# Kernel tuning notes

Hardware: AMD Instinct MI355X
Metric: run time of the kernel (lower is better)

The kernel has to match this reference:

```python
import jax, jax.numpy as jnp
import numpy as np

B, S, BITS = 1024, 4096, 32

# Boolean gates expressed as float arithmetic on {0,1} pulses (exact for 0/1 inputs,
# matching the SNN gate semantics: AND=a*b, OR=a+b-ab, NOT=1-a, XOR=a+b-2ab).

def _and(a, b):
    return a * b

def _or(a, b):
    return a + b - a * b

def _not(a):
    return 1.0 - a

def _xor(a, b):
    return a + b - 2.0 * a * b

def _full_adder(a, b, c):
    axb = _xor(a, b)
    s = _xor(axb, c)
    # carry = (a AND b) OR ((a XOR b) AND c); the two terms are disjoint for booleans
    carry = a * b + axb * c
    return s, carry


def setup_inputs() -> dict:
    key = jax.random.key(0)
    # FP32 bit-pulses: x[..., 0]=sign, x[..., 1:9]=exponent (MSB first), x[..., 9:32]=mantissa
    x = jax.random.bernoulli(key, 0.5, (B, S, BITS)).astype(jnp.float32)
    return {"x": x}


def reference(x):
    e_x = x[..., 1:9]    # exponent bits, MSB first  [.., 8]
    m_x = x[..., 9:32]   # mantissa bits, MSB first  [.., 23]
    ones = jnp.ones(x.shape[:-1] + (1,), dtype=x.dtype)

    # shift = e_x - 127 via ripple subtract: e + NOT(127) + 1.
    # NOT(127) in MSB-first 8-bit is [1,0,0,0,0,0,0,0].
    borrow = ones
    shift = [None] * 8
    for i in range(7, -1, -1):
        nb = 1.0 if i == 0 else 0.0
        s, borrow = _full_adder(e_x[..., i:i + 1], nb, borrow)
        shift[i] = s
    s_bits = shift                      # MSB first
    s_inv = [_not(b) for b in s_bits]

    # high 5 bits (s0..s4) all zero
    hi_zero = s_inv[0]
    for i in range(1, 5):
        hi_zero = _and(hi_zero, s_inv[i])

    is_0 = _and(hi_zero, _and(s_inv[5], _and(s_inv[6], s_inv[7])))
    is_1 = _and(hi_zero, _and(s_inv[5], _and(s_inv[6], s_bits[7])))
    is_2 = _and(hi_zero, _and(s_inv[5], _and(s_bits[6], s_inv[7])))
    is_3 = _and(hi_zero, _and(s_inv[5], _and(s_bits[6], s_bits[7])))
    is_4 = _and(hi_zero, _and(s_bits[5], _and(s_inv[6], s_inv[7])))
    is_s = [is_0, is_1, is_2, is_3, is_4]

    m = [m_x[..., i:i + 1] for i in range(4)]  # top 4 mantissa bits (MSB first)

    final_bits = []
    for b in range(5):
        terms = []
        for s in range(5):
            if s == b:
                terms.append(_and(is_s[s], ones))
            elif s > b:
                m_idx = s - 1 - b
                if m_idx < 4:
                    terms.append(_and(is_s[s], m[m_idx]))
        res = terms[0]
        for i in range(1, len(terms)):
            res = _or(res, terms[i])
        final_bits.append(res)

    # output MSB first: [b4, b3, b2, b1, b0]
    return jnp.concatenate(list(reversed(final_bits)), axis=-1)
```

## Files before the change

kernel.cpp:

```cpp
#include <hip/hip_runtime.h>


#define BIT(u) (((u) >> 23) & 1u)

__global__ __launch_bounds__(256) void spike_kernel(
    const uint4* __restrict__ in, uint4* __restrict__ out)
{
    __shared__ unsigned int obuf[5120];

    const int t   = threadIdx.x;
    const int sub = t & 3;
    const int egq = t >> 2;
    const size_t blk_e0 = (size_t)blockIdx.x * 1024;

    const int nib_shift     = (3 - sub) * 4;
    const int out_bit_shift = 4 - sub;

#pragma unroll
    for (int i = 0; i < 16; ++i) {
        const int e_local = i * 64 + egq;
        uint4 u = in[(blk_e0 + e_local) * 8 + sub];

        unsigned int nib = (BIT(u.x) << 3) | (BIT(u.y) << 2) |
                           (BIT(u.z) << 1) |  BIT(u.w);
        int V = (int)(nib << nib_shift);
        V |= __builtin_amdgcn_mov_dpp(V, 0xB1, 0xF, 0xF, true);
        V |= __builtin_amdgcn_mov_dpp(V, 0x4E, 0xF, 0xF, true);
        unsigned int Vu = (unsigned int)V;
        unsigned int eint  = (Vu >> 7) & 0xFFu;
        unsigned int mant  = (Vu >> 3) & 0xFu;
        unsigned int shift = (eint + 129u) & 255u;
        unsigned int mb    = 16u | mant;
        unsigned int val5  = (shift <= 4u) ? (mb >> (4u - shift)) : 0u;

        unsigned int* ob = &obuf[e_local * 5];
        ob[sub] = (0u - ((val5 >> out_bit_shift) & 1u)) & 0x3f800000u;
        if (sub == 0)
            ob[4] = (0u - (val5 & 1u)) & 0x3f800000u;
    }

    __syncthreads();

    const uint4* ob4 = (const uint4*)obuf;
    uint4* q = out + (size_t)blockIdx.x * 1280;
#pragma unroll
    for (int k = 0; k < 5; ++k)
        q[k * 256 + t] = ob4[k * 256 + t];
}

extern "C" void kernel_launch(void* const* d_in, const int* in_sizes, int n_in,
                              void* d_out, int out_size, void* d_ws, size_t ws_size,
                              hipStream_t stream) {
    (void)n_in; (void)d_ws; (void)ws_size; (void)out_size;
    const uint4* in = (const uint4*)d_in[0];
    uint4* out = (uint4*)d_out;

    int n_elem = in_sizes[0] / 32;
    int grid   = n_elem / 1024;
    spike_kernel<<<grid, 256, 0, stream>>>(in, out);
}
```

Baseline: 124.8 us.

## Load full contiguous elements and batch eight loads per thread

Threads now read every 16-byte chunk of each 128-byte element, so each wave load instruction covers one contiguous 1 KB span. Each thread issues eight loads before any compute, which puts more memory requests in flight. Lanes holding the unused chunks only skip the shared-memory write. The cost is fetching input bytes the result never uses, which helps only if the hardware already moved whole cache lines before, plus more registers held per thread.

```diff
diff --git a/kernel.cpp b/kernel.cpp
--- a/kernel.cpp
+++ b/kernel.cpp
@@ -8,35 +8,45 @@
 {
     __shared__ unsigned int obuf[5120];
 
-    const int t   = threadIdx.x;
-    const int sub = t & 3;
-    const int egq = t >> 2;
-    const size_t blk_e0 = (size_t)blockIdx.x * 1024;
+    const int t    = threadIdx.x;
+    const int lane = t & 63;
+    const int w    = t >> 6;
+    const int sub  = lane & 7;
+    const int g    = lane >> 3;
+    const size_t blk_u4 = (size_t)blockIdx.x * 8192;
 
-    const int nib_shift     = (3 - sub) * 4;
-    const int out_bit_shift = 4 - sub;
+    const bool active    = (sub < 4);
+    const int  nib_shift = (3 - (sub & 3)) * 4;
 
 #pragma unroll
-    for (int i = 0; i < 16; ++i) {
-        const int e_local = i * 64 + egq;
-        uint4 u = in[(blk_e0 + e_local) * 8 + sub];
+    for (int m = 0; m < 4; ++m) {
+        uint4 v[8];
+#pragma unroll
+        for (int k = 0; k < 8; ++k)
+            v[k] = in[blk_u4 + (size_t)m * 2048 + w * 512 + k * 64 + lane];
 
-        unsigned int nib = (BIT(u.x) << 3) | (BIT(u.y) << 2) |
-                           (BIT(u.z) << 1) |  BIT(u.w);
-        int V = (int)(nib << nib_shift);
-        V |= __builtin_amdgcn_mov_dpp(V, 0xB1, 0xF, 0xF, true);
-        V |= __builtin_amdgcn_mov_dpp(V, 0x4E, 0xF, 0xF, true);
-        unsigned int Vu = (unsigned int)V;
-        unsigned int eint  = (Vu >> 7) & 0xFFu;
-        unsigned int mant  = (Vu >> 3) & 0xFu;
-        unsigned int shift = (eint + 129u) & 255u;
-        unsigned int mb    = 16u | mant;
-        unsigned int val5  = (shift <= 4u) ? (mb >> (4u - shift)) : 0u;
+#pragma unroll
+        for (int k = 0; k < 8; ++k) {
+            uint4 u = v[k];
+            unsigned int nib = (BIT(u.x) << 3) | (BIT(u.y) << 2) |
+                               (BIT(u.z) << 1) |  BIT(u.w);
+            int V = (int)(nib << nib_shift);
+            V |= __builtin_amdgcn_mov_dpp(V, 0xB1, 0xF, 0xF, true);
+            V |= __builtin_amdgcn_mov_dpp(V, 0x4E, 0xF, 0xF, true);
+            unsigned int Vu = (unsigned int)V;
+            unsigned int eint  = (Vu >> 7) & 0xFFu;
+            unsigned int mant  = (Vu >> 3) & 0xFu;
+            unsigned int shift = (eint + 129u) & 255u;
+            unsigned int val5  = (shift <= 4u) ? ((16u | mant) >> (4u - shift)) : 0u;
 
-        unsigned int* ob = &obuf[e_local * 5];
-        ob[sub] = (0u - ((val5 >> out_bit_shift) & 1u)) & 0x3f800000u;
-        if (sub == 0)
-            ob[4] = (0u - (val5 & 1u)) & 0x3f800000u;
+            if (active) {
+                int em = m * 256 + w * 64 + k * 8 + g;
+                unsigned int* ob = &obuf[em * 5];
+                ob[sub] = (0u - ((val5 >> (4 - sub)) & 1u)) & 0x3f800000u;
+                if (sub == 0)
+                    ob[4] = (0u - (val5 & 1u)) & 0x3f800000u;
+            }
+        }
     }
 
     __syncthreads();
@@ -44,8 +54,8 @@
     const uint4* ob4 = (const uint4*)obuf;
     uint4* q = out + (size_t)blockIdx.x * 1280;
 #pragma unroll
-    for (int k = 0; k < 5; ++k)
-        q[k * 256 + t] = ob4[k * 256 + t];
+    for (int kk = 0; kk < 5; ++kk)
+        q[kk * 256 + t] = ob4[kk * 256 + t];
 }
 
 extern "C" void kernel_launch(void* const* d_in, const int* in_sizes, int n_in,
```

Result: no change. 126.2 us (+1.1%).
